# Kernel tuning notes

Hardware: AMD Instinct MI355X
Metric: run time of the kernel (lower is better)

The kernel has to match this reference:

```python
import jax, jax.numpy as jnp
import numpy as np

ALPHA = 0.2  # LeakyReLU negative slope


def setup_inputs() -> dict:
    key = jax.random.key(0)
    k1, k2, k3, k4, k5 = jax.random.split(key, 5)
    n, fin, fout = 4096, 512, 512
    X = jax.random.normal(k1, (n, fin), dtype=jnp.float32)
    # sparse-ish 0/1 adjacency with self loops so every softmax row is non-empty
    A = (jax.random.uniform(k2, (n, n)) < 0.005).astype(jnp.float32)
    A = jnp.minimum(A + jnp.eye(n, dtype=jnp.float32), 1.0)
    W_short = jax.random.normal(k3, (fout, fin), dtype=jnp.float32) * 0.02
    r = jax.random.normal(k4, (2 * fout, 1), dtype=jnp.float32) * 0.02
    W_long = jax.random.normal(k5, (fout, fin), dtype=jnp.float32) * 0.02
    return dict(X=X, A=A, W_short=W_short, r=r, W_long=W_long, num_hops=3)


def reference(X, A, W_short, r, W_long, num_hops):
    fout = W_short.shape[0]
    neg_inf = jnp.finfo(X.dtype).min

    # ---- ShortDistanceAttention ----
    Wh = X @ W_short.T                                   # (n, fout)
    # r^T [Wh_i || Wh_j] = (Wh_i . r_src) + (Wh_j . r_dst)
    src = Wh @ r[:fout, 0]                               # (n,)
    dst = Wh @ r[fout:, 0]                               # (n,)
    e = jax.nn.leaky_relu(src[:, None] + dst[None, :], ALPHA)  # (n, n)
    edge_mask = A != 0
    att = jax.nn.softmax(jnp.where(edge_mask, e, neg_inf), axis=1)
    hk = jax.nn.gelu(att @ Wh)                           # (n, fout)

    # ---- LongDistanceAttention ----
    Wa = X @ W_long.T                                    # (n, fout)
    # multi-hop reachability: union of nonzero patterns of A^1..A^num_hops
    Ak = A
    reach = A
    for _ in range(num_hops - 1):
        Ak = Ak @ A                                      # dense n^3 matmul
        reach = reach + Ak
    hop_mask = reach != 0
    scores = hk @ Wa.T                                   # (n, n)
    att2 = jax.nn.softmax(jnp.where(hop_mask, scores, neg_inf), axis=1)
    ok = att2 @ hk                                       # (n, fout)
    return ok
```

## Files before the change

### kernel.cpp

```cpp
#include <hip/hip_runtime.h>
#include <math.h>


#define N_NODES 4096
#define FDIM    512
#define MAX_NNZ 128
#define LRELU_ALPHA 0.2f
#define NUM_HOPS 3

typedef unsigned short ushort_t;
typedef unsigned long long u64;
typedef __attribute__((ext_vector_type(8))) __bf16 bf16x8;
typedef __attribute__((ext_vector_type(8))) _Float16 f16x8;
typedef __attribute__((ext_vector_type(4))) float f32x4;
typedef __attribute__((ext_vector_type(16))) float f32x16;

__device__ __forceinline__ ushort_t f2bf(float x) {
    unsigned u = __float_as_uint(x);
    u += 0x7fff + ((u >> 16) & 1);
    return (ushort_t)(u >> 16);
}
__device__ __forceinline__ float bf2f(ushort_t h) {
    return __uint_as_float((unsigned)h << 16);
}
__device__ __forceinline__ void split2(float x, ushort_t& h, ushort_t& l) {
    h = f2bf(x);
    l = f2bf(x - bf2f(h));
}
__device__ __forceinline__ ushort_t f2h(float x) {
    _Float16 v = (_Float16)x;
    return *(ushort_t*)&v;
}

__device__ __forceinline__ float gelu_tanh(float x) {
    float x3 = x * x * x;
    float t  = tanhf(0.7978845608028654f * (x + 0.044715f * x3));
    return 0.5f * x * (1.0f + t);
}

__device__ __forceinline__ void gload_lds16(const void* g, void* l) {
    __builtin_amdgcn_global_load_lds(
        (const __attribute__((address_space(1))) unsigned int*)g,
        (__attribute__((address_space(3))) unsigned int*)l, 16, 0, 0);
}

__global__ __launch_bounds__(256) void split_hl(const float* __restrict__ src,
                                                ushort_t* __restrict__ h,
                                                ushort_t* __restrict__ l, int n) {
    int i = blockIdx.x * 256 + threadIdx.x;
    int stride = gridDim.x * 256;
    for (; i < n; i += stride) {
        ushort_t hh, ll;
        split2(src[i], hh, ll);
        h[i] = hh; l[i] = ll;
    }
}

__global__ __launch_bounds__(256) void transpose_f16(const float* __restrict__ src,
                                                     ushort_t* __restrict__ tf) {
    __shared__ float tile[32][33];
    int bx = blockIdx.x;
    int by = blockIdx.y;
    int tx = threadIdx.x & 31;
    int ty = threadIdx.x >> 5;
    for (int r = ty; r < 32; r += 8)
        tile[r][tx] = src[(size_t)(by * 32 + r) * FDIM + bx * 32 + tx];
    __syncthreads();
    for (int r = ty; r < 32; r += 8) {
        float v = tile[tx][r];
        tf[(size_t)(bx * 32 + r) * N_NODES + by * 32 + tx] = f2h(v);
    }
}

template <int BM, int BN>
__global__ __launch_bounds__(256) void gemm_f16(
    const ushort_t* __restrict__ Af, int lda,
    const ushort_t* __restrict__ Bf, int ldb,
    float* __restrict__ Cf, int ldc, int M, int N, int Klen) {
    constexpr int WTN = BN / 2;
    constexpr int JT  = WTN / 32;

    __shared__ ushort_t As[BM * 32];
    __shared__ ushort_t Bs[BN * 32];

    int t = threadIdx.x;
    int wave = t >> 6, lane = t & 63;
    int wr = wave >> 1, wc = wave & 1;
    int row0 = blockIdx.y * BM, col0 = blockIdx.x * BN;
    int kb = blockIdx.z * Klen;
    Cf += (size_t)blockIdx.z * M * ldc;

    f32x16 acc[2][JT] = {};
    int m32 = lane & 31;
    int e   = lane >> 5;

    int rr = t >> 2;
    int cs = (t & 3) ^ ((t >> 3) & 3);
    const ushort_t* pA[BM / 64];
    const ushort_t* pB[BN / 64];
#pragma unroll
    for (int q = 0; q < BM / 64; q++)
        pA[q] = Af + (size_t)(row0 + q * 64 + rr) * lda + kb + cs * 8;
#pragma unroll
    for (int q = 0; q < BN / 64; q++)
        pB[q] = Bf + (size_t)(col0 + q * 64 + rr) * ldb + kb + cs * 8;

    for (int ks = 0; ks < Klen; ks += 32) {
#pragma unroll
        for (int q = 0; q < BM / 64; q++) {
            gload_lds16(pA[q], As + (q * 256 + wave * 64) * 8);
            pA[q] += 32;
        }
#pragma unroll
        for (int q = 0; q < BN / 64; q++) {
            gload_lds16(pB[q], Bs + (q * 256 + wave * 64) * 8);
            pB[q] += 32;
        }
        __syncthreads();

        f16x8 af[2][2], bf[JT][2];
#pragma unroll
        for (int i = 0; i < 2; i++) {
            int ar = wr * 64 + i * 32 + m32;
            int sw = (ar >> 1) & 3;
#pragma unroll
            for (int kh = 0; kh < 2; kh++) {
                int slot = (kh * 2 + e) ^ sw;
                af[i][kh] = *(const f16x8*)(As + ar * 32 + slot * 8);
            }
        }
#pragma unroll
        for (int j = 0; j < JT; j++) {
            int bc = wc * WTN + j * 32 + m32;
            int sw = (bc >> 1) & 3;
#pragma unroll
            for (int kh = 0; kh < 2; kh++) {
                int slot = (kh * 2 + e) ^ sw;
                bf[j][kh] = *(const f16x8*)(Bs + bc * 32 + slot * 8);
            }
        }
#pragma unroll
        for (int i = 0; i < 2; i++)
#pragma unroll
            for (int j = 0; j < JT; j++)
#pragma unroll
                for (int kh = 0; kh < 2; kh++)
                    acc[i][j] = __builtin_amdgcn_mfma_f32_32x32x16_f16(af[i][kh], bf[j][kh], acc[i][j], 0, 0, 0);
        __syncthreads();
    }

    int rbase = 4 * e;
#pragma unroll
    for (int i = 0; i < 2; i++)
#pragma unroll
        for (int j = 0; j < JT; j++) {
            int col = col0 + wc * WTN + j * 32 + m32;
#pragma unroll
            for (int rg = 0; rg < 16; rg++) {
                int row = row0 + wr * 64 + i * 32 + (rg & 3) + 8 * (rg >> 2) + rbase;
                Cf[(size_t)row * ldc + col] = acc[i][j][rg];
            }
        }
}

template <int BM, int BN>
__global__ __launch_bounds__(256) void gemm3_nt(
    const ushort_t* __restrict__ Ah, const ushort_t* __restrict__ Al, int lda,
    const ushort_t* __restrict__ Bh, const ushort_t* __restrict__ Bl, int ldb,
    float* __restrict__ Cf, int ldc, int Klen, ushort_t* __restrict__ Ef) {
    constexpr int WTN = BN / 2;
    constexpr int JT  = WTN / 32;

    __shared__ ushort_t As_h[BM * 32], As_l[BM * 32];
    __shared__ ushort_t Bs_h[BN * 32], Bs_l[BN * 32];

    int t = threadIdx.x;
    int wave = t >> 6, lane = t & 63;
    int wr = wave >> 1, wc = wave & 1;
    int row0 = blockIdx.y * BM, col0 = blockIdx.x * BN;

    f32x16 acc[2][JT] = {};
    int m32 = lane & 31;
    int e   = lane >> 5;

    int rr = t >> 2;
    int cs = (t & 3) ^ ((t >> 3) & 3);
    const ushort_t* pAh[BM / 64];
    const ushort_t* pAl[BM / 64];
    const ushort_t* pBh[BN / 64];
    const ushort_t* pBl[BN / 64];
#pragma unroll
    for (int q = 0; q < BM / 64; q++) {
        size_t o = (size_t)(row0 + q * 64 + rr) * lda + cs * 8;
        pAh[q] = Ah + o; pAl[q] = Al + o;
    }
#pragma unroll
    for (int q = 0; q < BN / 64; q++) {
        size_t o = (size_t)(col0 + q * 64 + rr) * ldb + cs * 8;
        pBh[q] = Bh + o; pBl[q] = Bl + o;
    }

    for (int ks = 0; ks < Klen; ks += 32) {
#pragma unroll
        for (int q = 0; q < BM / 64; q++) {
            int ldsoff = (q * 256 + wave * 64) * 8;
            gload_lds16(pAh[q], As_h + ldsoff);
            gload_lds16(pAl[q], As_l + ldsoff);
            pAh[q] += 32; pAl[q] += 32;
        }
#pragma unroll
        for (int q = 0; q < BN / 64; q++) {
            int ldsoff = (q * 256 + wave * 64) * 8;
            gload_lds16(pBh[q], Bs_h + ldsoff);
            gload_lds16(pBl[q], Bs_l + ldsoff);
            pBh[q] += 32; pBl[q] += 32;
        }
        __syncthreads();

        bf16x8 afh[2][2], afl[2][2], bfh[JT][2], bfl[JT][2];
#pragma unroll
        for (int i = 0; i < 2; i++) {
            int ar = wr * 64 + i * 32 + m32;
            int sw = (ar >> 1) & 3;
#pragma unroll
            for (int kh = 0; kh < 2; kh++) {
                int slot = (kh * 2 + e) ^ sw;
                afh[i][kh] = *(const bf16x8*)(As_h + ar * 32 + slot * 8);
                afl[i][kh] = *(const bf16x8*)(As_l + ar * 32 + slot * 8);
            }
        }
#pragma unroll
        for (int j = 0; j < JT; j++) {
            int bc = wc * WTN + j * 32 + m32;
            int sw = (bc >> 1) & 3;
#pragma unroll
            for (int kh = 0; kh < 2; kh++) {
                int slot = (kh * 2 + e) ^ sw;
                bfh[j][kh] = *(const bf16x8*)(Bs_h + bc * 32 + slot * 8);
                bfl[j][kh] = *(const bf16x8*)(Bs_l + bc * 32 + slot * 8);
            }
        }
#pragma unroll
        for (int i = 0; i < 2; i++)
#pragma unroll
            for (int j = 0; j < JT; j++)
#pragma unroll
                for (int kh = 0; kh < 2; kh++) {
                    acc[i][j] = __builtin_amdgcn_mfma_f32_32x32x16_bf16(afh[i][kh], bfh[j][kh], acc[i][j], 0, 0, 0);
                    acc[i][j] = __builtin_amdgcn_mfma_f32_32x32x16_bf16(afh[i][kh], bfl[j][kh], acc[i][j], 0, 0, 0);
                    acc[i][j] = __builtin_amdgcn_mfma_f32_32x32x16_bf16(afl[i][kh], bfh[j][kh], acc[i][j], 0, 0, 0);
                }
        __syncthreads();
    }

    int rbase = 4 * e;
#pragma unroll
    for (int i = 0; i < 2; i++)
#pragma unroll
        for (int j = 0; j < JT; j++) {
            int col = col0 + wc * WTN + j * 32 + m32;
#pragma unroll
            for (int rg = 0; rg < 16; rg++) {
                int row = row0 + wr * 64 + i * 32 + (rg & 3) + 8 * (rg >> 2) + rbase;
                float v = acc[i][j][rg];
                if (col < FDIM)
                    Cf[(size_t)row * ldc + col] = v;
                else
                    Ef[(size_t)row * FDIM + col - FDIM] = f2h(v);
            }
        }
}

__global__ __launch_bounds__(256) void reduce4(const f32x4* __restrict__ P,
                                               f32x4* __restrict__ out) {
    const size_t stride = (size_t)N_NODES * FDIM / 4;
    int i = blockIdx.x * 256 + threadIdx.x;
    out[i] = P[i] + P[i + stride] + P[i + 2 * stride] + P[i + 3 * stride];
}

__global__ __launch_bounds__(256) void srcdst_kernel(const float* __restrict__ Wh,
                                                     const float* __restrict__ r,
                                                     float* __restrict__ src,
                                                     float* __restrict__ dst) {
    int i = blockIdx.x, t = threadIdx.x;
    float ps = 0.0f, pd = 0.0f;
    for (int k = t; k < FDIM; k += 256) {
        float w = Wh[(size_t)i * FDIM + k];
        ps += w * r[k];
        pd += w * r[FDIM + k];
    }
    __shared__ float sbuf[512];
    sbuf[t] = ps; sbuf[256 + t] = pd;
    __syncthreads();
    for (int s = 128; s > 0; s >>= 1) {
        if (t < s) { sbuf[t] += sbuf[t + s]; sbuf[256 + t] += sbuf[256 + t + s]; }
        __syncthreads();
    }
    if (t == 0) { src[i] = sbuf[0]; dst[i] = sbuf[256]; }
}

__global__ __launch_bounds__(256) void prep_A(const float* __restrict__ A,
                                              int* __restrict__ nnz,
                                              int* __restrict__ idx,
                                              u64* __restrict__ bits,
                                              u64* __restrict__ reach) {
    int i = blockIdx.x, t = threadIdx.x;
    int wave = t >> 6, lane = t & 63;
    __shared__ int cnt;
    if (t == 0) cnt = 0;
    __syncthreads();
    for (int w = wave; w < 64; w += 4) {
        float a = A[(size_t)i * N_NODES + w * 64 + lane];
        bool nz = a != 0.0f;
        u64 m = __ballot(nz);
        if (lane == 0) { bits[i * 64 + w] = m; reach[i * 64 + w] = m; }
        if (nz) {
            int s = atomicAdd(&cnt, 1);
            if (s < MAX_NNZ) idx[i * MAX_NNZ + s] = w * 64 + lane;
        }
    }
    __syncthreads();
    if (t == 0) nnz[i] = cnt < MAX_NNZ ? cnt : MAX_NNZ;
}

__global__ __launch_bounds__(256) void hop_kernel(const u64* __restrict__ in,
                                                  u64* __restrict__ out,
                                                  u64* __restrict__ reach,
                                                  const int* __restrict__ nnz,
                                                  const int* __restrict__ idx) {
    int i = blockIdx.x * 4 + (threadIdx.x >> 6);
    int w = threadIdx.x & 63;
    int cnt = nnz[i];
    u64 acc = 0ULL;
    for (int q = 0; q < cnt; q++) {
        int j = idx[i * MAX_NNZ + q];
        acc |= in[(size_t)j * 64 + w];
    }
    out[i * 64 + w] = acc;
    reach[i * 64 + w] |= acc;
}

__global__ __launch_bounds__(256) void short_attn(const float* __restrict__ Wh,
                                                  const float* __restrict__ src,
                                                  const float* __restrict__ dst,
                                                  const int* __restrict__ nnz,
                                                  const int* __restrict__ idx,
                                                  float* __restrict__ hk,
                                                  ushort_t* __restrict__ hkf) {
    int i = blockIdx.x, t = threadIdx.x;
    __shared__ int   s_idx[MAX_NNZ];
    __shared__ float s_w[MAX_NNZ];
    __shared__ float s_m, s_sum;
    int cnt = nnz[i];
    float si = src[i];
    if (t < cnt) {
        int j = idx[i * MAX_NNZ + t];
        s_idx[t] = j;
        float e = si + dst[j];
        s_w[t] = e > 0.0f ? e : LRELU_ALPHA * e;
    }
    __syncthreads();
    if (t == 0) {
        float m = -INFINITY;
        for (int q = 0; q < cnt; q++) m = fmaxf(m, s_w[q]);
        s_m = m;
    }
    __syncthreads();
    if (t < cnt) s_w[t] = __expf(s_w[t] - s_m);
    __syncthreads();
    if (t == 0) {
        float s = 0.0f;
        for (int q = 0; q < cnt; q++) s += s_w[q];
        s_sum = s;
    }
    __syncthreads();
    float inv = 1.0f / s_sum;
    const float2* W2 = (const float2*)Wh;
    float ax = 0.0f, ay = 0.0f;
    for (int q = 0; q < cnt; q++) {
        float w = s_w[q];
        float2 v = W2[(size_t)s_idx[q] * (FDIM / 2) + t];
        ax += w * v.x; ay += w * v.y;
    }
    float vx = gelu_tanh(ax * inv);
    float vy = gelu_tanh(ay * inv);
    size_t o = (size_t)i * FDIM + 2 * t;
    hk[o] = vx; hk[o + 1] = vy;
    hkf[o] = f2h(vx); hkf[o + 1] = f2h(vy);
}

__global__ __launch_bounds__(256) void long_softmax_f16(float* __restrict__ scores,
                                                        const u64* __restrict__ reach) {
    int i = blockIdx.x, t = threadIdx.x;
    __shared__ u64 sw[64];
    __shared__ float red[256];
    if (t < 64) sw[t] = reach[i * 64 + t];
    float* g = scores + (size_t)i * N_NODES;
    float v[16];
    bool on[16];
    __syncthreads();
    float m = -INFINITY;
#pragma unroll
    for (int q = 0; q < 16; q++) {
        int j = q * 256 + t;
        v[q] = g[j];
        on[q] = (sw[j >> 6] >> (j & 63)) & 1ULL;
        if (on[q]) m = fmaxf(m, v[q]);
    }
    red[t] = m; __syncthreads();
    for (int s = 128; s > 0; s >>= 1) {
        if (t < s) red[t] = fmaxf(red[t], red[t + s]);
        __syncthreads();
    }
    m = red[0]; __syncthreads();
    float sum = 0.0f;
#pragma unroll
    for (int q = 0; q < 16; q++) {
        float p = on[q] ? __expf(v[q] - m) : 0.0f;
        v[q] = p;
        sum += p;
    }
    red[t] = sum; __syncthreads();
    for (int s = 128; s > 0; s >>= 1) {
        if (t < s) red[t] += red[t + s];
        __syncthreads();
    }
    float inv = 1.0f / red[0];
    ushort_t* outf = (ushort_t*)g;
#pragma unroll
    for (int q = 0; q < 16; q++) {
        int j = q * 256 + t;
        outf[j] = f2h(v[q] * inv);
    }
}

extern "C" void kernel_launch(void* const* d_in, const int* in_sizes, int n_in,
                              void* d_out, int out_size, void* d_ws, size_t ws_size,
                              hipStream_t stream) {
    (void)in_sizes; (void)n_in; (void)out_size; (void)ws_size;
    const float* X       = (const float*)d_in[0];
    const float* A       = (const float*)d_in[1];
    const float* W_short = (const float*)d_in[2];
    const float* r       = (const float*)d_in[3];
    const float* W_long  = (const float*)d_in[4];

    char* p = (char*)d_ws;
    float* scores = (float*)p;   p += (size_t)N_NODES * N_NODES * 4;
    float* Psplit = (float*)p;   p += (size_t)4 * N_NODES * FDIM * 4;
    float* Wh     = (float*)p;   p += (size_t)N_NODES * FDIM * 4;
    float* hk     = (float*)p;   p += (size_t)N_NODES * FDIM * 4;
    ushort_t* Xh  = (ushort_t*)p; p += (size_t)N_NODES * FDIM * 2;
    ushort_t* Xl  = (ushort_t*)p; p += (size_t)N_NODES * FDIM * 2;
    ushort_t* Waf = (ushort_t*)p; p += (size_t)N_NODES * FDIM * 2;
    ushort_t* Wch = (ushort_t*)p; p += (size_t)1024 * FDIM * 2;
    ushort_t* Wcl = (ushort_t*)p; p += (size_t)1024 * FDIM * 2;
    int* idx      = (int*)p;     p += (size_t)N_NODES * MAX_NNZ * 4;
    u64* Abits    = (u64*)p;     p += (size_t)N_NODES * 64 * 8;
    u64* Bcur     = (u64*)p;     p += (size_t)N_NODES * 64 * 8;
    u64* Bnxt     = (u64*)p;     p += (size_t)N_NODES * 64 * 8;
    u64* reach    = (u64*)p;     p += (size_t)N_NODES * 64 * 8;
    float* src    = (float*)p;   p += N_NODES * 4;
    float* dst    = (float*)p;   p += N_NODES * 4;
    int* nnz      = (int*)p;     p += N_NODES * 4;

    ushort_t* hkf   = Xh;
    ushort_t* hkTf  = (ushort_t*)Wh;
    ushort_t* att2f = (ushort_t*)scores;

    split_hl<<<2048, 256, 0, stream>>>(X, Xh, Xl, N_NODES * FDIM);
    split_hl<<<512, 256, 0, stream>>>(W_short, Wch, Wcl, FDIM * FDIM);
    split_hl<<<512, 256, 0, stream>>>(W_long, Wch + (size_t)FDIM * FDIM,
                                      Wcl + (size_t)FDIM * FDIM, FDIM * FDIM);

    gemm3_nt<128, 64><<<dim3(1024 / 64, N_NODES / 128), 256, 0, stream>>>(
        Xh, Xl, FDIM, Wch, Wcl, FDIM, Wh, FDIM, FDIM, Waf);

    srcdst_kernel<<<N_NODES, 256, 0, stream>>>(Wh, r, src, dst);

    prep_A<<<N_NODES, 256, 0, stream>>>(A, nnz, idx, Abits, reach);
    const u64* in_b = Abits;
    u64* out_b = Bcur;
    for (int h = 0; h < NUM_HOPS - 1; h++) {
        hop_kernel<<<N_NODES / 4, 256, 0, stream>>>(in_b, out_b, reach, nnz, idx);
        in_b = out_b;
        out_b = (out_b == Bcur) ? Bnxt : Bcur;
    }

    short_attn<<<N_NODES, 256, 0, stream>>>(Wh, src, dst, nnz, idx, hk, hkf);

    transpose_f16<<<dim3(FDIM / 32, N_NODES / 32), 256, 0, stream>>>(hk, hkTf);

    gemm_f16<128, 128><<<dim3(N_NODES / 128, N_NODES / 128, 1), 256, 0, stream>>>(
        hkf, FDIM, Waf, FDIM, scores, N_NODES, N_NODES, N_NODES, FDIM);

    long_softmax_f16<<<N_NODES, 256, 0, stream>>>(scores, reach);

    gemm_f16<128, 128><<<dim3(FDIM / 128, N_NODES / 128, 4), 256, 0, stream>>>(
        att2f, 2 * N_NODES, hkTf, N_NODES, Psplit, FDIM, N_NODES, FDIM, N_NODES / 4);
    reduce4<<<2048, 256, 0, stream>>>((const f32x4*)Psplit, (f32x4*)d_out);
}
```

Baseline: 333.2 us.

## Store scores as fp16, fuse split kernels, drop fp32 hk, swizzle split-K grid

The score GEMM now writes fp16 directly instead of fp32, which halves the traffic of the 4096x4096 score matrix. The softmax reads and writes that fp16 buffer in place with vectorized 16-byte accesses. The three split_hl launches become one float4-vectorized kernel. The fp32 hk buffer is removed, so the transpose now works on the fp16 copy. The final split-K GEMM uses a 1D grid with a block-index swizzle to improve L2 reuse. The price is that the pre-softmax scores are rounded to fp16, which loses range and precision.

```diff
diff --git a/kernel.cpp b/kernel.cpp
--- a/kernel.cpp
+++ b/kernel.cpp
@@ -44,21 +44,36 @@
         (__attribute__((address_space(3))) unsigned int*)l, 16, 0, 0);
 }
 
-__global__ __launch_bounds__(256) void split_hl(const float* __restrict__ src,
-                                                ushort_t* __restrict__ h,
-                                                ushort_t* __restrict__ l, int n) {
+__global__ __launch_bounds__(256) void split_all(const float4* __restrict__ X,
+                                                 const float4* __restrict__ Ws,
+                                                 const float4* __restrict__ Wl,
+                                                 ushort4* __restrict__ Xh,
+                                                 ushort4* __restrict__ Xl,
+                                                 ushort4* __restrict__ Wch,
+                                                 ushort4* __restrict__ Wcl) {
+    const int n0 = N_NODES * FDIM / 4;
+    const int n1 = FDIM * FDIM / 4;
+    const int total = n0 + 2 * n1;
     int i = blockIdx.x * 256 + threadIdx.x;
     int stride = gridDim.x * 256;
-    for (; i < n; i += stride) {
-        ushort_t hh, ll;
-        split2(src[i], hh, ll);
-        h[i] = hh; l[i] = ll;
-    }
-}
-
-__global__ __launch_bounds__(256) void transpose_f16(const float* __restrict__ src,
+    for (; i < total; i += stride) {
+        float4 v;
+        ushort4* dh;
+        ushort4* dl;
+        int o;
+        if (i < n0)               { v = X[i];            dh = Xh;  dl = Xl;  o = i; }
+        else if (i < n0 + n1)     { o = i - n0;          v = Ws[o]; dh = Wch; dl = Wcl; }
+        else                      { o = i - n0 - n1;     v = Wl[o]; dh = Wch + n1; dl = Wcl + n1; o = o; }
+        ushort4 h, l;
+        split2(v.x, h.x, l.x); split2(v.y, h.y, l.y);
+        split2(v.z, h.z, l.z); split2(v.w, h.w, l.w);
+        dh[o] = h; dl[o] = l;
+    }
+}
+
+__global__ __launch_bounds__(256) void transpose_f16(const ushort_t* __restrict__ src,
                                                      ushort_t* __restrict__ tf) {
-    __shared__ float tile[32][33];
+    __shared__ ushort_t tile[32][33];
     int bx = blockIdx.x;
     int by = blockIdx.y;
     int tx = threadIdx.x & 31;
@@ -66,29 +81,40 @@
     for (int r = ty; r < 32; r += 8)
         tile[r][tx] = src[(size_t)(by * 32 + r) * FDIM + bx * 32 + tx];
     __syncthreads();
-    for (int r = ty; r < 32; r += 8) {
-        float v = tile[tx][r];
-        tf[(size_t)(bx * 32 + r) * N_NODES + by * 32 + tx] = f2h(v);
-    }
+    for (int r = ty; r < 32; r += 8)
+        tf[(size_t)(bx * 32 + r) * N_NODES + by * 32 + tx] = tile[tx][r];
 }
 
 template <int BM, int BN>
 __global__ __launch_bounds__(256) void gemm_f16(
     const ushort_t* __restrict__ Af, int lda,
     const ushort_t* __restrict__ Bf, int ldb,
-    float* __restrict__ Cf, int ldc, int M, int N, int Klen) {
+    float* __restrict__ Cf, ushort_t* __restrict__ CfH, int ldc,
+    int M, int N, int Klen, int swz) {
     constexpr int WTN = BN / 2;
     constexpr int JT  = WTN / 32;
 
     __shared__ ushort_t As[BM * 32];
     __shared__ ushort_t Bs[BN * 32];
+
+    int bx, by, bz;
+    if (swz) {
+        int bid = blockIdx.x;
+        int r8 = bid & 7, q = bid >> 3;
+        bx = q & 3;
+        int w = q >> 2;
+        int yz = (w << 3) | r8;
+        by = yz & 31; bz = yz >> 5;
+    } else {
+        bx = blockIdx.x; by = blockIdx.y; bz = blockIdx.z;
+    }
 
     int t = threadIdx.x;
     int wave = t >> 6, lane = t & 63;
     int wr = wave >> 1, wc = wave & 1;
-    int row0 = blockIdx.y * BM, col0 = blockIdx.x * BN;
-    int kb = blockIdx.z * Klen;
-    Cf += (size_t)blockIdx.z * M * ldc;
+    int row0 = by * BM, col0 = bx * BN;
+    int kb = bz * Klen;
+    if (!CfH) Cf += (size_t)bz * M * ldc;
 
     f32x16 acc[2][JT] = {};
     int m32 = lane & 31;
@@ -158,7 +184,8 @@
 #pragma unroll
             for (int rg = 0; rg < 16; rg++) {
                 int row = row0 + wr * 64 + i * 32 + (rg & 3) + 8 * (rg >> 2) + rbase;
-                Cf[(size_t)row * ldc + col] = acc[i][j][rg];
+                if (CfH) CfH[(size_t)row * ldc + col] = f2h(acc[i][j][rg]);
+                else     Cf[(size_t)row * ldc + col] = acc[i][j][rg];
             }
         }
 }
@@ -345,7 +372,6 @@
                                                   const float* __restrict__ dst,
                                                   const int* __restrict__ nnz,
                                                   const int* __restrict__ idx,
-                                                  float* __restrict__ hk,
                                                   ushort_t* __restrict__ hkf) {
     int i = blockIdx.x, t = threadIdx.x;
     __shared__ int   s_idx[MAX_NNZ];
@@ -385,27 +411,31 @@
     float vx = gelu_tanh(ax * inv);
     float vy = gelu_tanh(ay * inv);
     size_t o = (size_t)i * FDIM + 2 * t;
-    hk[o] = vx; hk[o + 1] = vy;
     hkf[o] = f2h(vx); hkf[o + 1] = f2h(vy);
 }
 
-__global__ __launch_bounds__(256) void long_softmax_f16(float* __restrict__ scores,
-                                                        const u64* __restrict__ reach) {
+__global__ __launch_bounds__(256) void long_softmax_f16ip(ushort_t* __restrict__ scoresF,
+                                                          const u64* __restrict__ reach) {
     int i = blockIdx.x, t = threadIdx.x;
     __shared__ u64 sw[64];
     __shared__ float red[256];
     if (t < 64) sw[t] = reach[i * 64 + t];
-    float* g = scores + (size_t)i * N_NODES;
+    f16x8* row = (f16x8*)(scoresF + (size_t)i * N_NODES);
     float v[16];
-    bool on[16];
+    unsigned onbits = 0;
     __syncthreads();
     float m = -INFINITY;
 #pragma unroll
-    for (int q = 0; q < 16; q++) {
-        int j = q * 256 + t;
-        v[q] = g[j];
-        on[q] = (sw[j >> 6] >> (j & 63)) & 1ULL;
-        if (on[q]) m = fmaxf(m, v[q]);
+    for (int u = 0; u < 2; u++) {
+        f16x8 a = row[2 * t + u];
+#pragma unroll
+        for (int k = 0; k < 8; k++) {
+            int q = u * 8 + k;
+            int j = (2 * t + u) * 8 + k;
+            v[q] = (float)a[k];
+            bool on = (sw[j >> 6] >> (j & 63)) & 1ULL;
+            if (on) { onbits |= 1u << q; m = fmaxf(m, v[q]); }
+        }
     }
     red[t] = m; __syncthreads();
     for (int s = 128; s > 0; s >>= 1) {
@@ -416,7 +446,7 @@
     float sum = 0.0f;
 #pragma unroll
     for (int q = 0; q < 16; q++) {
-        float p = on[q] ? __expf(v[q] - m) : 0.0f;
+        float p = (onbits >> q) & 1 ? __expf(v[q] - m) : 0.0f;
         v[q] = p;
         sum += p;
     }
@@ -426,11 +456,13 @@
         __syncthreads();
     }
     float inv = 1.0f / red[0];
-    ushort_t* outf = (ushort_t*)g;
-#pragma unroll
-    for (int q = 0; q < 16; q++) {
-        int j = q * 256 + t;
-        outf[j] = f2h(v[q] * inv);
+#pragma unroll
+    for (int u = 0; u < 2; u++) {
+        f16x8 o;
+#pragma unroll
+        for (int k = 0; k < 8; k++)
+            o[k] = (_Float16)(v[u * 8 + k] * inv);
+        row[2 * t + u] = o;
     }
 }
 
@@ -445,10 +477,9 @@
     const float* W_long  = (const float*)d_in[4];
 
     char* p = (char*)d_ws;
-    float* scores = (float*)p;   p += (size_t)N_NODES * N_NODES * 4;
+    ushort_t* scoresF = (ushort_t*)p; p += (size_t)N_NODES * N_NODES * 2;
     float* Psplit = (float*)p;   p += (size_t)4 * N_NODES * FDIM * 4;
     float* Wh     = (float*)p;   p += (size_t)N_NODES * FDIM * 4;
-    float* hk     = (float*)p;   p += (size_t)N_NODES * FDIM * 4;
     ushort_t* Xh  = (ushort_t*)p; p += (size_t)N_NODES * FDIM * 2;
     ushort_t* Xl  = (ushort_t*)p; p += (size_t)N_NODES * FDIM * 2;
     ushort_t* Waf = (ushort_t*)p; p += (size_t)N_NODES * FDIM * 2;
@@ -463,14 +494,13 @@
     float* dst    = (float*)p;   p += N_NODES * 4;
     int* nnz      = (int*)p;     p += N_NODES * 4;
 
-    ushort_t* hkf   = Xh;
-    ushort_t* hkTf  = (ushort_t*)Wh;
-    ushort_t* att2f = (ushort_t*)scores;
-
-    split_hl<<<2048, 256, 0, stream>>>(X, Xh, Xl, N_NODES * FDIM);
-    split_hl<<<512, 256, 0, stream>>>(W_short, Wch, Wcl, FDIM * FDIM);
-    split_hl<<<512, 256, 0, stream>>>(W_long, Wch + (size_t)FDIM * FDIM,
-                                      Wcl + (size_t)FDIM * FDIM, FDIM * FDIM);
+    ushort_t* hkf  = Xh;
+    ushort_t* hkTf = (ushort_t*)Wh;
+
+    split_all<<<1280, 256, 0, stream>>>((const float4*)X, (const float4*)W_short,
+                                        (const float4*)W_long,
+                                        (ushort4*)Xh, (ushort4*)Xl,
+                                        (ushort4*)Wch, (ushort4*)Wcl);
 
     gemm3_nt<128, 64><<<dim3(1024 / 64, N_NODES / 128), 256, 0, stream>>>(
         Xh, Xl, FDIM, Wch, Wcl, FDIM, Wh, FDIM, FDIM, Waf);
@@ -486,16 +516,17 @@
         out_b = (out_b == Bcur) ? Bnxt : Bcur;
     }
 
-    short_attn<<<N_NODES, 256, 0, stream>>>(Wh, src, dst, nnz, idx, hk, hkf);
-
-    transpose_f16<<<dim3(FDIM / 32, N_NODES / 32), 256, 0, stream>>>(hk, hkTf);
-
-    gemm_f16<128, 128><<<dim3(N_NODES / 128, N_NODES / 128, 1), 256, 0, stream>>>(
-        hkf, FDIM, Waf, FDIM, scores, N_NODES, N_NODES, N_NODES, FDIM);
-
-    long_softmax_f16<<<N_NODES, 256, 0, stream>>>(scores, reach);
-
-    gemm_f16<128, 128><<<dim3(FDIM / 128, N_NODES / 128, 4), 256, 0, stream>>>(
-        att2f, 2 * N_NODES, hkTf, N_NODES, Psplit, FDIM, N_NODES, FDIM, N_NODES / 4);
+    short_attn<<<N_NODES, 256, 0, stream>>>(Wh, src, dst, nnz, idx, hkf);
+
+    transpose_f16<<<dim3(FDIM / 32, N_NODES / 32), 256, 0, stream>>>(hkf, hkTf);
+
+    gemm_f16<128, 128><<<dim3(N_NODES / 128, N_NODES / 128), 256, 0, stream>>>(
+        hkf, FDIM, Waf, FDIM, nullptr, scoresF, N_NODES, N_NODES, N_NODES, FDIM, 0);
+
+    long_softmax_f16ip<<<N_NODES, 256, 0, stream>>>(scoresF, reach);
+
+    gemm_f16<128, 128><<<512, 256, 0, stream>>>(
+        scoresF, N_NODES, hkTf, N_NODES, Psplit, nullptr, FDIM,
+        N_NODES, FDIM, N_NODES / 4, 1);
     reduce4<<<2048, 256, 0, stream>>>((const f32x4*)Psplit, (f32x4*)d_out);
 }
```

New measurement: 295.5 us. -11.3%, faster.
